# Kernel tuning notes

Hardware: AMD Instinct MI355X
Metric: run time of the kernel (lower is better)

Reference implementation:

```python
import jax, jax.numpy as jnp
import numpy as np

K = 2  # n_experts_per_tok (init kwarg)


def setup_inputs() -> dict:
    key = jax.random.key(0)
    ks = jax.random.split(key, 11)
    B, S, D, E, SH, F = 2, 4096, 2048, 8, 2, 512
    sc = 0.02
    return {
        "x": jax.random.normal(ks[0], (B, S, D), jnp.float32),
        "router_w": jax.random.normal(ks[1], (E, D), jnp.float32) * sc,
        "router_b": jax.random.normal(ks[2], (E,), jnp.float32) * sc,
        "ew1": jax.random.normal(ks[3], (E, D, F), jnp.float32) * sc,
        "eb1": jax.random.normal(ks[4], (E, F), jnp.float32) * sc,
        "ew2": jax.random.normal(ks[5], (E, F, D), jnp.float32) * sc,
        "eb2": jax.random.normal(ks[6], (E, D), jnp.float32) * sc,
        "sw1": jax.random.normal(ks[7], (SH, D, F), jnp.float32) * sc,
        "sb1": jax.random.normal(ks[8], (SH, F), jnp.float32) * sc,
        "sw2": jax.random.normal(ks[9], (SH, F, D), jnp.float32) * sc,
        "sb2": jax.random.normal(ks[10], (SH, D), jnp.float32) * sc,
    }


def reference(x, router_w, router_b, ew1, eb1, ew2, eb2, sw1, sb1, sw2, sb2):
    B, S, D = x.shape
    E = ew1.shape[0]
    # Router + top-k gating
    logits = jnp.einsum("bsd,ed->bse", x, router_w) + router_b          # (B,S,E)
    topv, topi = jax.lax.top_k(logits, K)                                # (B,S,K)
    gates = jax.nn.softmax(topv, axis=-1)                                # (B,S,K)
    # Per-(token, expert) combine weight: sum over slots of gate * 1[idx==e]
    w = jnp.einsum("bsk,bske->bse", gates,
                   jax.nn.one_hot(topi, E, dtype=x.dtype))               # (B,S,E)
    # Routed experts: dense per-expert FFN (math identical to masked gather/scatter loop)
    h = jax.nn.gelu(jnp.einsum("bsd,edf->ebsf", x, ew1)
                    + eb1[:, None, None, :], approximate=False)          # (E,B,S,F)
    y = jnp.einsum("ebsf,efd->ebsd", h, ew2) + eb2[:, None, None, :]     # (E,B,S,D)
    out = jnp.einsum("ebsd,bse->bsd", y, w)                              # (B,S,D)
    # Shared experts (always active, ungated)
    hs = jax.nn.gelu(jnp.einsum("bsd,kdf->kbsf", x, sw1)
                     + sb1[:, None, None, :], approximate=False)
    ys = jnp.einsum("kbsf,kfd->kbsd", hs, sw2) + sb2[:, None, None, :]
    out = out + ys.sum(axis=0)
    # Load-balance aux loss (faithful to source, including its slot-vs-expert-id quirk)
    num_tokens = B * S
    flat = topi.reshape(-1, K)                                           # (N,K) int
    counts_k = jnp.sum(flat == jnp.arange(K)[None, :], axis=0).astype(jnp.float32)
    expert_counts = jnp.zeros((E,), jnp.float32).at[:K].set(counts_k)
    expert_counts = expert_counts / (num_tokens * K) + 1e-8
    load_balance_loss = -jnp.sum(expert_counts * jnp.log(expert_counts))
    return out, load_balance_loss
```

## Files before the change

### kernel.cpp

```cpp
#include <hip/hip_runtime.h>
#include <hip/hip_bf16.h>
#include <cstdint>

#define TOKENS   8192
#define D_DIM    2048
#define F_DIM    512
#define NE       8
#define NSH      2
#define NZ       10
#define OUT_ELEMS (TOKENS * D_DIM)

#define RCAP     17408
#define SH_BASE  RCAP
#define NPAIRS   (RCAP + 2 * TOKENS)
#define MAX_RT   136
#define G1_CAP   320
#define G2R_CAP  1024

typedef __attribute__((ext_vector_type(8))) short bf16x8;
typedef __attribute__((ext_vector_type(4))) float f32x4;

__device__ __forceinline__ short f2bf(float f) {
  union { float f; uint32_t u; } v; v.f = f;
  uint32_t r = (v.u + 0x7fffu + ((v.u >> 16) & 1u)) >> 16;
  return (short)r;
}
__device__ __forceinline__ float bf2f(short s) {
  union { float f; uint32_t u; } v; v.u = ((uint32_t)(uint16_t)s) << 16; return v.f;
}

__device__ __forceinline__ void gload_lds16(const void* g, void* l) {
  __builtin_amdgcn_global_load_lds(
      (const __attribute__((address_space(1))) unsigned int*)g,
      (__attribute__((address_space(3))) unsigned int*)l,
      16, 0, 0);
}

__global__ void k_transpose(const float* __restrict__ ein,
                            const float* __restrict__ sin_,
                            short* __restrict__ out, int R, int C) {
  __shared__ float tile[32][33];
  int b = blockIdx.z;
  const float* in = (b < NE) ? (ein + (size_t)b * R * C)
                             : (sin_ + (size_t)(b - NE) * R * C);
  out += (size_t)b * R * C;
  int c0 = blockIdx.x * 32, r0 = blockIdx.y * 32;
  #pragma unroll
  for (int i = 0; i < 32; i += 8) {
    int r = r0 + threadIdx.y + i, c = c0 + threadIdx.x;
    tile[threadIdx.y + i][threadIdx.x] = in[(size_t)r * C + c];
  }
  __syncthreads();
  #pragma unroll
  for (int i = 0; i < 32; i += 8) {
    int c = c0 + threadIdx.y + i, r = r0 + threadIdx.x;
    out[(size_t)c * R + r] = f2bf(tile[threadIdx.x][threadIdx.y + i]);
  }
}

__global__ __launch_bounds__(256) void k_router(
    const float* __restrict__ x, const float* __restrict__ rw,
    const float* __restrict__ rb, short* __restrict__ xb,
    int2* __restrict__ ti, float2* __restrict__ tg) {
  int wave = threadIdx.x >> 6;
  int lane = threadIdx.x & 63;
  int t = blockIdx.x * 4 + wave;
  const float4* xr = (const float4*)(x + (size_t)t * D_DIM);
  short4* xbr = (short4*)(xb + (size_t)t * D_DIM);
  const float4* rw4 = (const float4*)rw;
  float acc[NE];
  #pragma unroll
  for (int e = 0; e < NE; e++) acc[e] = 0.f;
  #pragma unroll
  for (int it = 0; it < D_DIM / 4 / 64; it++) {
    int i = it * 64 + lane;
    float4 v = xr[i];
    short4 o;
    o.x = f2bf(v.x); o.y = f2bf(v.y); o.z = f2bf(v.z); o.w = f2bf(v.w);
    xbr[i] = o;
    #pragma unroll
    for (int e = 0; e < NE; e++) {
      float4 w = rw4[e * (D_DIM / 4) + i];
      acc[e] += v.x * w.x + v.y * w.y + v.z * w.z + v.w * w.w;
    }
  }
  #pragma unroll
  for (int e = 0; e < NE; e++) {
    #pragma unroll
    for (int off = 32; off > 0; off >>= 1) acc[e] += __shfl_xor(acc[e], off);
  }
  if (lane == 0) {
    float lg[NE];
    #pragma unroll
    for (int e = 0; e < NE; e++) lg[e] = acc[e] + rb[e];
    int i0 = 0;
    #pragma unroll
    for (int e = 1; e < NE; e++) if (lg[e] > lg[i0]) i0 = e;
    int i1 = (i0 == 0) ? 1 : 0;
    #pragma unroll
    for (int e = 0; e < NE; e++) if (e != i0 && e != i1 && lg[e] > lg[i1]) i1 = e;
    float e1 = __expf(lg[i1] - lg[i0]);
    float inv = 1.f / (1.f + e1);
    ti[t] = make_int2(i0, i1);
    tg[t] = make_float2(inv, e1 * inv);
  }
}

__global__ __launch_bounds__(1024) void k_count(
    const int2* __restrict__ ti, int* __restrict__ meta,
    int* __restrict__ tile_z, int* __restrict__ tile_row,
    int* __restrict__ pair_tok, float* __restrict__ pair_gate,
    float* __restrict__ out_loss) {
  __shared__ int cnt[NE + 2];
  if (threadIdx.x < NE + 2) cnt[threadIdx.x] = 0;
  for (int i = threadIdx.x; i < RCAP; i += 1024) {
    pair_tok[i] = 0; pair_gate[i] = 0.f;
  }
  __syncthreads();
  int loc[NE]; int l0 = 0, l1 = 0;
  #pragma unroll
  for (int e = 0; e < NE; e++) loc[e] = 0;
  for (int t = threadIdx.x; t < TOKENS; t += 1024) {
    int2 ii = ti[t];
    loc[ii.x]++; loc[ii.y]++;
    l0 += (ii.x == 0); l1 += (ii.y == 1);
  }
  #pragma unroll
  for (int e = 0; e < NE; e++) if (loc[e]) atomicAdd(&cnt[e], loc[e]);
  if (l0) atomicAdd(&cnt[NE], l0);
  if (l1) atomicAdd(&cnt[NE + 1], l1);
  __syncthreads();
  if (threadIdx.x == 0) {
    int base = 0, nrt = 0;
    #pragma unroll
    for (int e = 0; e < NE; e++) {
      int c = cnt[e];
      meta[e] = c;
      meta[19 + e] = base;
      meta[8 + e] = 0;
      int nt = (c + 127) >> 7;
      meta[40 + e] = nrt;
      meta[48 + e] = nt;
      for (int i = 0; i < nt; i++) { tile_z[nrt] = e; tile_row[nrt] = base + i * 128; nrt++; }
      base += nt * 128;
    }
    meta[18] = nrt;
    for (int i = 0; i < 128; i++) {
      tile_z[MAX_RT + i] = NE + (i >> 6);
      tile_row[MAX_RT + i] = SH_BASE + (i >> 6) * TOKENS + (i & 63) * 128;
    }
    float p0 = (float)cnt[NE] / 16384.0f + 1e-8f;
    float p1 = (float)cnt[NE + 1] / 16384.0f + 1e-8f;
    float rest = 6.0f * (1e-8f * logf(1e-8f));
    out_loss[0] = -(p0 * logf(p0) + p1 * logf(p1) + rest);
  }
}

__global__ __launch_bounds__(256) void k_assign(
    const int2* __restrict__ ti, const float2* __restrict__ tg,
    int* __restrict__ meta, int* __restrict__ pair_tok, float* __restrict__ pair_gate,
    int2* __restrict__ pos) {
  int t = blockIdx.x * 256 + threadIdx.x;
  int lane = threadIdx.x & 63;
  int2 ii = ti[t];
  float2 gg = tg[t];
  int2 mypos;
  unsigned long long below = (1ull << lane) - 1ull;
  #pragma unroll
  for (int e = 0; e < NE; e++) {
    unsigned long long m0 = __ballot(ii.x == e);
    unsigned long long m1 = __ballot(ii.y == e);
    unsigned c = __popcll(m0) + __popcll(m1);
    unsigned base = 0;
    if (lane == 0 && c) base = atomicAdd((unsigned*)&meta[8 + e], c);
    base = __shfl((int)base, 0);
    int seg = meta[19 + e];
    if (ii.x == e) {
      int p = seg + base + __popcll(m0 & below);
      pair_tok[p] = t; pair_gate[p] = gg.x; mypos.x = p;
    }
    if (ii.y == e) {
      int p = seg + base + __popcll(m0) + __popcll(m1 & below);
      pair_tok[p] = t; pair_gate[p] = gg.y; mypos.y = p;
    }
  }
  pos[t] = mypos;
  pair_tok[SH_BASE + t] = t;            pair_gate[SH_BASE + t] = 1.f;
  pair_tok[SH_BASE + TOKENS + t] = t;   pair_gate[SH_BASE + TOKENS + t] = 1.f;
}


#define FRAGS_MFMA(BUF_)                                                  \
    __builtin_amdgcn_s_setprio(1);                                        \
    _Pragma("unroll") for (int kk = 0; kk < 2; kk++) {                    \
      const int slt = kk ? slt1 : slt0;                                   \
      bf16x8 af[4], bfr[4];                                               \
      _Pragma("unroll") for (int m = 0; m < 4; m++) {                     \
        af[m]  = *(const bf16x8*)&As[BUF_][rowAo[m] + slt];               \
        bfr[m] = *(const bf16x8*)&Bs[BUF_][rowBo[m] + slt];               \
      }                                                                   \
      _Pragma("unroll") for (int m = 0; m < 4; m++)                       \
        _Pragma("unroll") for (int n = 0; n < 4; n++)                     \
          acc[m][n] = __builtin_amdgcn_mfma_f32_16x16x32_bf16(            \
              af[m], bfr[n], acc[m][n], 0, 0, 0);                         \
    }                                                                     \
    __builtin_amdgcn_s_setprio(0);

#define GBODY(T_, BUF_, NTV, STAGE_MACRO)                                 \
    if ((T_) + 1 < (NTV)) asm volatile("s_waitcnt vmcnt(8)" ::: "memory");\
    else                  asm volatile("s_waitcnt vmcnt(0)" ::: "memory");\
    __builtin_amdgcn_s_barrier();                                         \
    asm volatile("" ::: "memory");                                        \
    FRAGS_MFMA(BUF_);                                                     \
    if ((T_) + 2 < (NTV)) {                                               \
      asm volatile("s_waitcnt lgkmcnt(0)" ::: "memory");                  \
      __builtin_amdgcn_s_barrier();                                       \
      asm volatile("" ::: "memory");                                      \
      STAGE_MACRO(BUF_, (T_) + 2);                                        \
    }

__global__ __launch_bounds__(256, 2) void k_gemm1(
    const short* __restrict__ xb, const short* __restrict__ w1t,
    const float* __restrict__ eb1, const float* __restrict__ sb1,
    const int* __restrict__ meta, const int* __restrict__ tile_z,
    const int* __restrict__ tile_row, const int* __restrict__ pair_tok,
    const float* __restrict__ pair_gate, short* __restrict__ H) {
  const int l = blockIdx.x;
  const int xcd = l & 7;
  const int i = l >> 3;
  const int ntx = meta[48 + xcd];
  int slot, bn;
  if (i < ntx * 4) {
    slot = meta[40 + xcd] + (i >> 2); bn = i & 3;
  } else {
    int j = i - ntx * 4;
    if (j >= 64) return;
    int js = xcd * 64 + j;
    slot = MAX_RT + (js >> 2); bn = js & 3;
  }
  const int z = tile_z[slot];
  const int row0 = tile_row[slot];
  __shared__ __align__(16) short As[2][8192];
  __shared__ __align__(16) short Bs[2][8192];
  const int tid = threadIdx.x;
  const int lane = tid & 63;
  const int wv = tid >> 6;
  const int wm = wv >> 1, wn = wv & 1;

  const short* asrc[4]; const short* bsrc[4];
  {
    const short* wb = w1t + (size_t)z * F_DIM * D_DIM;
    int shtok = 0;
    if (slot >= MAX_RT) {
      shtok = row0 - SH_BASE;
      if (shtok >= TOKENS) shtok -= TOKENS;
    }
    #pragma unroll
    for (int i2 = 0; i2 < 4; i2++) {
      int id = i2 * 256 + tid;
      int row = id >> 3, c = id & 7;
      int kc = ((c ^ (row & 7)) << 3);
      int arow = (slot < MAX_RT) ? pair_tok[row0 + row] : (shtok + row);
      asrc[i2] = xb + (size_t)arow * D_DIM + kc;
      bsrc[i2] = wb + (size_t)(bn * 128 + row) * D_DIM + kc;
    }
  }

  const int slt0 = (((lane >> 4)) ^ (lane & 7)) << 3;
  const int slt1 = ((4 + (lane >> 4)) ^ (lane & 7)) << 3;
  int rowAo[4], rowBo[4];
  #pragma unroll
  for (int m = 0; m < 4; m++) {
    rowAo[m] = (wm * 64 + m * 16 + (lane & 15)) * 64;
    rowBo[m] = (wn * 64 + m * 16 + (lane & 15)) * 64;
  }

  f32x4 acc[4][4];
  #pragma unroll
  for (int m = 0; m < 4; m++)
    #pragma unroll
    for (int n = 0; n < 4; n++) acc[m][n] = (f32x4)(0.f);

  #define STAGE1(BUF, TT) do {                                            \
      int k0_ = (TT) * 64;                                                \
      _Pragma("unroll") for (int i2 = 0; i2 < 4; i2++) {                  \
        int id_ = i2 * 256 + tid;                                         \
        gload_lds16(asrc[i2] + k0_, &As[BUF][id_ * 8]);                   \
        gload_lds16(bsrc[i2] + k0_, &Bs[BUF][id_ * 8]);                   \
      }                                                                   \
    } while (0)

  STAGE1(0, 0);
  STAGE1(1, 1);

  const int NT = D_DIM / 64;
  for (int t = 0; t < NT; t += 2) {
    GBODY(t,     0, NT, STAGE1);
    GBODY(t + 1, 1, NT, STAGE1);
  }
  #undef STAGE1

  const float* b1 = (z < NE) ? (eb1 + z * F_DIM) : (sb1 + (size_t)(z - NE) * F_DIM);
  #pragma unroll
  for (int m = 0; m < 4; m++) {
    #pragma unroll
    for (int r = 0; r < 4; r++) {
      int row = wm * 64 + m * 16 + (lane >> 4) * 4 + r;
      float g = pair_gate[row0 + row];
      #pragma unroll
      for (int n = 0; n < 4; n++) {
        int col = bn * 128 + wn * 64 + n * 16 + (lane & 15);
        float c = acc[m][n][r] + b1[col];
        float h = 0.5f * c * (1.0f + erff(c * 0.70710678118654752440f));
        H[(size_t)(row0 + row) * F_DIM + col] = f2bf(h * g);
      }
    }
  }
}

__global__ __launch_bounds__(256, 2) void k_gemm2r(
    const short* __restrict__ Hb, const short* __restrict__ w2t,
    const int* __restrict__ meta, const int* __restrict__ tile_z,
    const int* __restrict__ tile_row, short* __restrict__ Yr) {
  const int l = blockIdx.x;
  const int xcd = l & 7;
  const int i = l >> 3;
  const int ntx = meta[48 + xcd];
  if (i >= ntx * 16) return;
  const int slot = meta[40 + xcd] + (i >> 4);
  const int bn = i & 15;
  const int z = tile_z[slot];
  const int row0 = tile_row[slot];
  __shared__ __align__(16) short As[2][8192];
  __shared__ __align__(16) short Bs[2][8192];
  const int tid = threadIdx.x;
  const int lane = tid & 63;
  const int wv = tid >> 6;
  const int wm = wv >> 1, wn = wv & 1;

  const short* asrc[4]; const short* bsrc[4];
  {
    const short* Bb = w2t + (size_t)z * D_DIM * F_DIM;
    #pragma unroll
    for (int i2 = 0; i2 < 4; i2++) {
      int id = i2 * 256 + tid;
      int row = id >> 3, c = id & 7;
      int kc = ((c ^ (row & 7)) << 3);
      asrc[i2] = Hb + (size_t)(row0 + row) * F_DIM + kc;
      bsrc[i2] = Bb + (size_t)(bn * 128 + row) * F_DIM + kc;
    }
  }

  const int slt0 = (((lane >> 4)) ^ (lane & 7)) << 3;
  const int slt1 = ((4 + (lane >> 4)) ^ (lane & 7)) << 3;
  int rowAo[4], rowBo[4];
  #pragma unroll
  for (int m = 0; m < 4; m++) {
    rowAo[m] = (wm * 64 + m * 16 + (lane & 15)) * 64;
    rowBo[m] = (wn * 64 + m * 16 + (lane & 15)) * 64;
  }

  f32x4 acc[4][4];
  #pragma unroll
  for (int m = 0; m < 4; m++)
    #pragma unroll
    for (int n = 0; n < 4; n++) acc[m][n] = (f32x4)(0.f);

  #define STAGE2R(BUF, TT) do {                                           \
      int k0_ = (TT) * 64;                                                \
      _Pragma("unroll") for (int i2 = 0; i2 < 4; i2++) {                  \
        int id_ = i2 * 256 + tid;                                         \
        gload_lds16(asrc[i2] + k0_, &As[BUF][id_ * 8]);                   \
        gload_lds16(bsrc[i2] + k0_, &Bs[BUF][id_ * 8]);                   \
      }                                                                   \
    } while (0)

  STAGE2R(0, 0);
  STAGE2R(1, 1);

  const int NT = F_DIM / 64;
  for (int t = 0; t < NT; t += 2) {
    GBODY(t,     0, NT, STAGE2R);
    GBODY(t + 1, 1, NT, STAGE2R);
  }
  #undef STAGE2R

  #pragma unroll
  for (int m = 0; m < 4; m++) {
    #pragma unroll
    for (int r = 0; r < 4; r++) {
      int row = wm * 64 + m * 16 + (lane >> 4) * 4 + r;
      #pragma unroll
      for (int n = 0; n < 4; n++) {
        int col = bn * 128 + wn * 64 + n * 16 + (lane & 15);
        Yr[(size_t)(row0 + row) * D_DIM + col] = f2bf(acc[m][n][r]);
      }
    }
  }
}

__global__ __launch_bounds__(256, 2) void k_gemm2s(
    const short* __restrict__ Hb, const short* __restrict__ w2t,
    const int2* __restrict__ ti, const float2* __restrict__ tg,
    const float* __restrict__ eb2, const float* __restrict__ sb2,
    const short* __restrict__ Yr, const int2* __restrict__ pos,
    float* __restrict__ out) {
  const int l = blockIdx.x;
  const int js = (l & 7) * 128 + (l >> 3);
  const int t0 = (js >> 4) * 128;
  const int bn = js & 15;
  __shared__ __align__(16) short As[2][8192];
  __shared__ __align__(16) short Bs[2][8192];
  const int tid = threadIdx.x;
  const int lane = tid & 63;
  const int wv = tid >> 6;
  const int wm = wv >> 1, wn = wv & 1;

  size_t aoff[4], boff[4];
  #pragma unroll
  for (int i2 = 0; i2 < 4; i2++) {
    int id = i2 * 256 + tid;
    int row = id >> 3, c = id & 7;
    int kc = ((c ^ (row & 7)) << 3);
    aoff[i2] = (size_t)row * F_DIM + kc;
    boff[i2] = (size_t)(bn * 128 + row) * F_DIM + kc;
  }
  const short* Abase0 = Hb + (size_t)(SH_BASE + t0) * F_DIM;
  const short* Bbase0 = w2t + (size_t)NE * D_DIM * F_DIM;

  const int slt0 = (((lane >> 4)) ^ (lane & 7)) << 3;
  const int slt1 = ((4 + (lane >> 4)) ^ (lane & 7)) << 3;
  int rowAo[4], rowBo[4];
  #pragma unroll
  for (int m = 0; m < 4; m++) {
    rowAo[m] = (wm * 64 + m * 16 + (lane & 15)) * 64;
    rowBo[m] = (wn * 64 + m * 16 + (lane & 15)) * 64;
  }

  f32x4 acc[4][4];
  #pragma unroll
  for (int m = 0; m < 4; m++)
    #pragma unroll
    for (int n = 0; n < 4; n++) acc[m][n] = (f32x4)(0.f);

  #define STAGE2S(BUF, TT) do {                                           \
      int kcol_ = ((TT) * 64) & (F_DIM - 1);                              \
      const short* Ab_ = Abase0;                                          \
      const short* Bb_ = Bbase0;                                          \
      if ((TT) >= 8) {                                                    \
        Ab_ += (size_t)TOKENS * F_DIM;                                    \
        Bb_ += (size_t)D_DIM * F_DIM;                                     \
      }                                                                   \
      _Pragma("unroll") for (int i2 = 0; i2 < 4; i2++) {                  \
        int id_ = i2 * 256 + tid;                                         \
        gload_lds16(Ab_ + aoff[i2] + kcol_, &As[BUF][id_ * 8]);           \
        gload_lds16(Bb_ + boff[i2] + kcol_, &Bs[BUF][id_ * 8]);           \
      }                                                                   \
    } while (0)

  STAGE2S(0, 0);
  STAGE2S(1, 1);

  const int NT = 16;
  for (int t = 0; t < NT; t += 2) {
    GBODY(t,     0, NT, STAGE2S);
    GBODY(t + 1, 1, NT, STAGE2S);
  }
  #undef STAGE2S

  #pragma unroll
  for (int m = 0; m < 4; m++) {
    #pragma unroll
    for (int r = 0; r < 4; r++) {
      int row = t0 + wm * 64 + m * 16 + (lane >> 4) * 4 + r;
      int2 ii = ti[row]; float2 gg = tg[row];
      int2 p = pos[row];
      #pragma unroll
      for (int n = 0; n < 4; n++) {
        int col = bn * 128 + wn * 64 + n * 16 + (lane & 15);
        float v = acc[m][n][r]
                + gg.x * eb2[(size_t)ii.x * D_DIM + col]
                + gg.y * eb2[(size_t)ii.y * D_DIM + col]
                + sb2[col] + sb2[D_DIM + col]
                + bf2f(Yr[(size_t)p.x * D_DIM + col])
                + bf2f(Yr[(size_t)p.y * D_DIM + col]);
        out[(size_t)row * D_DIM + col] = v;
      }
    }
  }
}

extern "C" void kernel_launch(void* const* d_in, const int* in_sizes, int n_in,
                              void* d_out, int out_size, void* d_ws, size_t ws_size,
                              hipStream_t stream) {
  (void)in_sizes; (void)n_in; (void)out_size; (void)ws_size;
  const float* x        = (const float*)d_in[0];
  const float* router_w = (const float*)d_in[1];
  const float* router_b = (const float*)d_in[2];
  const float* ew1      = (const float*)d_in[3];
  const float* eb1      = (const float*)d_in[4];
  const float* ew2      = (const float*)d_in[5];
  const float* eb2      = (const float*)d_in[6];
  const float* sw1      = (const float*)d_in[7];
  const float* sb1      = (const float*)d_in[8];
  const float* sw2      = (const float*)d_in[9];
  const float* sb2      = (const float*)d_in[10];
  float* out = (float*)d_out;

  char* ws = (char*)d_ws;
  short*  w2t       = (short*)ws;
  short*  Hbuf      = w2t + (size_t)NZ * D_DIM * F_DIM;
  int2*   ti        = (int2*)(Hbuf + (size_t)NPAIRS * F_DIM);
  float2* tg        = (float2*)(ti + TOKENS);
  int2*   pos       = (int2*)(tg + TOKENS);
  int*    pair_tok  = (int*)(pos + TOKENS);
  float*  pair_gate = (float*)(pair_tok + NPAIRS);
  int*    meta      = (int*)(pair_gate + NPAIRS);
  int*    tile_z    = meta + 64;
  int*    tile_row  = tile_z + 512;
  short*  xb        = (short*)(((uintptr_t)(tile_row + 512) + 255) & ~(uintptr_t)255);
  short*  w1t       = xb + (size_t)TOKENS * D_DIM;
  short*  Yr        = xb;

  k_transpose<<<dim3(F_DIM / 32, D_DIM / 32, NZ), dim3(32, 8), 0, stream>>>(
      ew1, sw1, w1t, D_DIM, F_DIM);
  k_transpose<<<dim3(D_DIM / 32, F_DIM / 32, NZ), dim3(32, 8), 0, stream>>>(
      ew2, sw2, w2t, F_DIM, D_DIM);

  k_router<<<TOKENS / 4, 256, 0, stream>>>(x, router_w, router_b, xb, ti, tg);
  k_count<<<1, 1024, 0, stream>>>(ti, meta, tile_z, tile_row, pair_tok, pair_gate,
                                  out + OUT_ELEMS);
  k_assign<<<TOKENS / 256, 256, 0, stream>>>(ti, tg, meta, pair_tok, pair_gate, pos);

  k_gemm1<<<8 * G1_CAP, 256, 0, stream>>>(
      xb, w1t, eb1, sb1, meta, tile_z, tile_row, pair_tok, pair_gate, Hbuf);
  k_gemm2r<<<8 * G2R_CAP, 256, 0, stream>>>(
      Hbuf, w2t, meta, tile_z, tile_row, Yr);
  k_gemm2s<<<1024, 256, 0, stream>>>(
      Hbuf, w2t, ti, tg, eb2, sb2, Yr, pos, out);
}
```

Baseline: 339.5 us.

## Load all LDS fragments before barrier and issue next-stage copy before MFMAs

The GEMM main-loop body now reads both k-slices of A/B fragments from LDS up front, waits, syncs, and issues the global-to-LDS staging for tile T+2 before running the MFMA block. This lets the next prefetch overlap with the matrix math instead of waiting behind it, and removes one barrier per iteration. The cost is twice as many fragment registers live at once, which may raise register pressure at 2 waves per SIMD. Separately, zeroing of the routed pair buffers moves from the single-block count kernel into the wide router kernel, which shortens that serial step.

```diff
diff --git a/kernel.cpp b/kernel.cpp
--- a/kernel.cpp
+++ b/kernel.cpp
@@ -61,7 +61,10 @@
 __global__ __launch_bounds__(256) void k_router(
     const float* __restrict__ x, const float* __restrict__ rw,
     const float* __restrict__ rb, short* __restrict__ xb,
-    int2* __restrict__ ti, float2* __restrict__ tg) {
+    int2* __restrict__ ti, float2* __restrict__ tg,
+    int* __restrict__ pair_tok, float* __restrict__ pair_gate) {
+  int gid = blockIdx.x * 256 + threadIdx.x;
+  if (gid < RCAP) { pair_tok[gid] = 0; pair_gate[gid] = 0.f; }
   int wave = threadIdx.x >> 6;
   int lane = threadIdx.x & 63;
   int t = blockIdx.x * 4 + wave;
@@ -109,13 +112,9 @@
 __global__ __launch_bounds__(1024) void k_count(
     const int2* __restrict__ ti, int* __restrict__ meta,
     int* __restrict__ tile_z, int* __restrict__ tile_row,
-    int* __restrict__ pair_tok, float* __restrict__ pair_gate,
     float* __restrict__ out_loss) {
   __shared__ int cnt[NE + 2];
   if (threadIdx.x < NE + 2) cnt[threadIdx.x] = 0;
-  for (int i = threadIdx.x; i < RCAP; i += 1024) {
-    pair_tok[i] = 0; pair_gate[i] = 0.f;
-  }
   __syncthreads();
   int loc[NE]; int l0 = 0, l1 = 0;
   #pragma unroll
@@ -190,33 +189,34 @@
 }
 
 
-#define FRAGS_MFMA(BUF_)                                                  \
-    __builtin_amdgcn_s_setprio(1);                                        \
-    _Pragma("unroll") for (int kk = 0; kk < 2; kk++) {                    \
-      const int slt = kk ? slt1 : slt0;                                   \
-      bf16x8 af[4], bfr[4];                                               \
-      _Pragma("unroll") for (int m = 0; m < 4; m++) {                     \
-        af[m]  = *(const bf16x8*)&As[BUF_][rowAo[m] + slt];               \
-        bfr[m] = *(const bf16x8*)&Bs[BUF_][rowBo[m] + slt];               \
-      }                                                                   \
-      _Pragma("unroll") for (int m = 0; m < 4; m++)                       \
-        _Pragma("unroll") for (int n = 0; n < 4; n++)                     \
-          acc[m][n] = __builtin_amdgcn_mfma_f32_16x16x32_bf16(            \
-              af[m], bfr[n], acc[m][n], 0, 0, 0);                         \
-    }                                                                     \
-    __builtin_amdgcn_s_setprio(0);
-
 #define GBODY(T_, BUF_, NTV, STAGE_MACRO)                                 \
     if ((T_) + 1 < (NTV)) asm volatile("s_waitcnt vmcnt(8)" ::: "memory");\
     else                  asm volatile("s_waitcnt vmcnt(0)" ::: "memory");\
     __builtin_amdgcn_s_barrier();                                         \
     asm volatile("" ::: "memory");                                        \
-    FRAGS_MFMA(BUF_);                                                     \
-    if ((T_) + 2 < (NTV)) {                                               \
+    {                                                                     \
+      bf16x8 af0[4], bf0[4], af1[4], bf1[4];                              \
+      _Pragma("unroll") for (int m = 0; m < 4; m++) {                     \
+        af0[m] = *(const bf16x8*)&As[BUF_][rowAo[m] + slt0];              \
+        bf0[m] = *(const bf16x8*)&Bs[BUF_][rowBo[m] + slt0];              \
+        af1[m] = *(const bf16x8*)&As[BUF_][rowAo[m] + slt1];              \
+        bf1[m] = *(const bf16x8*)&Bs[BUF_][rowBo[m] + slt1];              \
+      }                                                                   \
       asm volatile("s_waitcnt lgkmcnt(0)" ::: "memory");                  \
+      __builtin_amdgcn_sched_barrier(0);                                  \
       __builtin_amdgcn_s_barrier();                                       \
       asm volatile("" ::: "memory");                                      \
-      STAGE_MACRO(BUF_, (T_) + 2);                                        \
+      if ((T_) + 2 < (NTV)) STAGE_MACRO(BUF_, (T_) + 2);                  \
+      __builtin_amdgcn_s_setprio(1);                                      \
+      _Pragma("unroll") for (int m = 0; m < 4; m++)                       \
+        _Pragma("unroll") for (int n = 0; n < 4; n++)                     \
+          acc[m][n] = __builtin_amdgcn_mfma_f32_16x16x32_bf16(            \
+              af0[m], bf0[n], acc[m][n], 0, 0, 0);                        \
+      _Pragma("unroll") for (int m = 0; m < 4; m++)                       \
+        _Pragma("unroll") for (int n = 0; n < 4; n++)                     \
+          acc[m][n] = __builtin_amdgcn_mfma_f32_16x16x32_bf16(            \
+              af1[m], bf1[n], acc[m][n], 0, 0, 0);                        \
+      __builtin_amdgcn_s_setprio(0);                                      \
     }
 
 __global__ __launch_bounds__(256, 2) void k_gemm1(
@@ -527,9 +527,9 @@
   k_transpose<<<dim3(D_DIM / 32, F_DIM / 32, NZ), dim3(32, 8), 0, stream>>>(
       ew2, sw2, w2t, F_DIM, D_DIM);
 
-  k_router<<<TOKENS / 4, 256, 0, stream>>>(x, router_w, router_b, xb, ti, tg);
-  k_count<<<1, 1024, 0, stream>>>(ti, meta, tile_z, tile_row, pair_tok, pair_gate,
-                                  out + OUT_ELEMS);
+  k_router<<<TOKENS / 4, 256, 0, stream>>>(x, router_w, router_b, xb, ti, tg,
+                                           pair_tok, pair_gate);
+  k_count<<<1, 1024, 0, stream>>>(ti, meta, tile_z, tile_row, out + OUT_ELEMS);
   k_assign<<<TOKENS / 256, 256, 0, stream>>>(ti, tg, meta, pair_tok, pair_gate, pos);
 
   k_gemm1<<<8 * G1_CAP, 256, 0, stream>>>(
```

Measured after the change: 334.9 us. No clear change (-1.3%).
